# Kernel tuning notes

Measured on AMD Instinct MI355X. Metric: run time of the kernel, lower is better.

Reference implementation:

```python
import jax, jax.numpy as jnp
import numpy as np
from jax import lax

B, L, T, H = 8192, 1024, 32, 32  # batch, input length, time steps, lstm hidden
EPS = 1e-5


def _conv1d(x, w, stride, pad):
    # x: [N, C, L], w: [O, I, K]
    return lax.conv_general_dilated(x, w, (stride,), [(pad, pad)],
                                    dimension_numbers=('NCH', 'OIH', 'NCH'))


def _bn(x, g, be, m, v):
    # eval-mode batchnorm over channel dim of [N, C, L]
    inv = g / jnp.sqrt(v + EPS)
    return x * inv[None, :, None] + (be - m * inv)[None, :, None]


def setup_inputs() -> dict:
    key = jax.random.key(0)
    ks = jax.random.split(key, 32)
    r = lambda i, shape, s=0.1: jax.random.normal(ks[i], shape, jnp.float32) * s
    u = lambda i, shape: jax.random.uniform(ks[i], shape, jnp.float32, 0.5, 1.5)
    return {
        'x': jax.random.normal(ks[0], (B, L, 1), jnp.float32),
        'w1': r(1, (8, 1, 7)), 'b1': r(2, (8,)), 'g1': u(3, (8,)), 'be1': r(4, (8,)),
        'm1': r(5, (8,)), 'v1': u(6, (8,)),
        'w2': r(7, (16, 8, 5)), 'b2': r(8, (16,)), 'g2': u(9, (16,)), 'be2': r(10, (16,)),
        'm2': r(11, (16,)), 'v2': u(12, (16,)),
        'w3': r(13, (32, 16, 3)), 'b3': r(14, (32,)), 'g3': u(15, (32,)), 'be3': r(16, (32,)),
        'm3': r(17, (32,)), 'v3': u(18, (32,)),
        'w_ih': r(19, (4 * H, 32)), 'w_hh': r(20, (4 * H, H)),
        'b_ih': r(21, (4 * H,)), 'b_hh': r(22, (4 * H,)),
        'fc1w': r(23, (64, 64)), 'fc1b': r(24, (64,)),
        'fc2w': r(25, (32, 64)), 'fc2b': r(26, (32,)),
        'fc3w': r(27, (4, 32)), 'fc3b': r(28, (4,)),
    }


def _forward(x, w1, b1, g1, be1, m1, v1, w2, b2, g2, be2, m2, v2,
             w3, b3, g3, be3, m3, v3, w_ih, w_hh, b_ih, b_hh,
             fc1w, fc1b, fc2w, fc2b, fc3w, fc3b):
    bsz = x.shape[0]
    h = x.transpose(0, 2, 1)                      # [B, 1, 1024]
    h = jax.nn.relu(_bn(_conv1d(h, w1, 4, 3) + b1[None, :, None], g1, be1, m1, v1))
    h = jax.nn.relu(_bn(_conv1d(h, w2, 4, 2) + b2[None, :, None], g2, be2, m2, v2))
    h = jax.nn.relu(_bn(_conv1d(h, w3, 2, 1) + b3[None, :, None], g3, be3, m3, v3))
    # h: [B, 32, 32]
    spatial = h.mean(axis=2)                      # [B, 32]
    snn_in = h.transpose(0, 2, 1).reshape(bsz, T, -1)  # [B, 32, 32]

    # LIF neuron: sequential decay/threshold/reset scan over time
    def lif_step(mem, xt):
        mem = 0.9 * mem + xt
        spike = (mem > 0.5).astype(xt.dtype)
        mem = mem * (1.0 - spike)
        return mem, spike

    _, spikes = lax.scan(lif_step, jnp.zeros((bsz, snn_in.shape[2]), snn_in.dtype),
                         snn_in.transpose(1, 0, 2))  # spikes: [T, B, F]

    # single-layer LSTM, keep only last hidden state
    def lstm_step(carry, xt):
        hh, cc = carry
        gates = xt @ w_ih.T + b_ih + hh @ w_hh.T + b_hh
        i, f, g, o = jnp.split(gates, 4, axis=1)
        cc = jax.nn.sigmoid(f) * cc + jax.nn.sigmoid(i) * jnp.tanh(g)
        hh = jax.nn.sigmoid(o) * jnp.tanh(cc)
        return (hh, cc), None

    init = (jnp.zeros((bsz, H), x.dtype), jnp.zeros((bsz, H), x.dtype))
    (h_last, _), _ = lax.scan(lstm_step, init, spikes)

    combined = jnp.concatenate([h_last, spatial], axis=1)  # [B, 64]
    z = jax.nn.relu(combined @ fc1w.T + fc1b)
    z = jax.nn.relu(z @ fc2w.T + fc2b)
    out = z @ fc3w.T + fc3b                                # [B, 4]
    return out, spatial, h_last


def reference(x, w1, b1, g1, be1, m1, v1, w2, b2, g2, be2, m2, v2,
              w3, b3, g3, be3, m3, v3, w_ih, w_hh, b_ih, b_hh,
              fc1w, fc1b, fc2w, fc2b, fc3w, fc3b):
    return _forward(x, w1, b1, g1, be1, m1, v1, w2, b2, g2, be2, m2, v2,
                    w3, b3, g3, be3, m3, v3, w_ih, w_hh, b_ih, b_hh,
                    fc1w, fc1b, fc2w, fc2b, fc3w, fc3b)
```

## Files before the change

kernel.cpp:

```cpp
#include <hip/hip_runtime.h>

#define NB 8192
#define EPS_BN 1e-5f

#define PADX(i) ((i) + ((((i) >> 5)) << 2))

using bf16x8 = __attribute__((ext_vector_type(8))) __bf16;
using bf16x4 = __attribute__((ext_vector_type(4))) __bf16;
using f32x4  = __attribute__((ext_vector_type(4))) float;
using f32x2  = __attribute__((ext_vector_type(2))) float;
using u32x4  = __attribute__((ext_vector_type(4))) unsigned int;

#define WSF_OFF 262144
#define PK_WIH  2560
#define PK_WHH  4608
#define PK_FC1  6656
#define PK_FC2  8704
#define PK_FC3  9728
#define PK_BFR  9984
#define PK_B1   10112
#define PK_B2   10176
#define PK_B3   10208
#define PK_SPB  12288

__device__ inline unsigned pack_bf16(float a, float b) {
    union { __bf16 h; unsigned short u; } ca, cb;
    ca.h = (__bf16)a; cb.h = (__bf16)b;
    return (unsigned)ca.u | ((unsigned)cb.u << 16);
}

__global__ __launch_bounds__(256) void fold_kernel(
    const float* __restrict__ w1, const float* __restrict__ b1,
    const float* __restrict__ g1, const float* __restrict__ be1,
    const float* __restrict__ m1, const float* __restrict__ v1,
    const float* __restrict__ w2, const float* __restrict__ b2,
    const float* __restrict__ g2, const float* __restrict__ be2,
    const float* __restrict__ m2, const float* __restrict__ v2,
    const float* __restrict__ w3, const float* __restrict__ b3,
    const float* __restrict__ g3, const float* __restrict__ be3,
    const float* __restrict__ m3, const float* __restrict__ v3,
    const float* __restrict__ w_ih, const float* __restrict__ w_hh,
    const float* __restrict__ b_ih, const float* __restrict__ b_hh,
    const float* __restrict__ fc1w, const float* __restrict__ fc1b,
    const float* __restrict__ fc2w, const float* __restrict__ fc2b,
    const float* __restrict__ fc3w, const float* __restrict__ fc3b,
    float* __restrict__ wsf)
{
    int j = blockIdx.x * 256 + threadIdx.x;
    if (j < 64) {
        int k = j >> 3, c = j & 7;
        wsf[j] = (k < 7) ? w1[c * 7 + k] * (g1[c] * rsqrtf(v1[c] + EPS_BN)) : 0.f;
    } else if (j < 72) {
        int c = j - 64;
        float inv = g1[c] * rsqrtf(v1[c] + EPS_BN);
        wsf[j] = (b1[c] - m1[c]) * inv + be1[c];
    } else if (j >= 80 && j < 720) {
        int i = j - 80, c = i & 15, t = i >> 4, ci = t / 5, k = t - 5 * ci;
        wsf[j] = w2[(c * 8 + ci) * 5 + k] * (g2[c] * rsqrtf(v2[c] + EPS_BN));
    } else if (j >= 720 && j < 736) {
        int c = j - 720;
        float inv = g2[c] * rsqrtf(v2[c] + EPS_BN);
        wsf[j] = (b2[c] - m2[c]) * inv + be2[c];
    } else if (j >= 736 && j < 2272) {
        int i = j - 736, c = i & 31, t = i >> 5, ci = t / 3, k = t - 3 * ci;
        wsf[j] = w3[(c * 16 + ci) * 3 + k] * (g3[c] * rsqrtf(v3[c] + EPS_BN));
    } else if (j >= 2272 && j < 2304) {
        int c = j - 2272;
        float inv = g3[c] * rsqrtf(v3[c] + EPS_BN);
        wsf[j] = (b3[c] - m3[c]) * inv + be3[c];
    } else if (j >= 2560 && j < 3072) {
        int idx = j - 2560, T = idx >> 6, j6 = idx & 63, row = j6 & 15, q = j6 >> 4;
        const float* src = w_ih + (size_t)(16 * T + row) * 32 + 8 * q;
        unsigned* dst = (unsigned*)(wsf + PK_WIH) + (size_t)idx * 4;
        #pragma unroll
        for (int i = 0; i < 4; i++) dst[i] = pack_bf16(src[2 * i], src[2 * i + 1]);
    } else if (j >= 3072 && j < 3584) {
        int idx = j - 3072, T = idx >> 6, j6 = idx & 63, row = j6 & 15, q = j6 >> 4;
        const float* src = w_hh + (size_t)(16 * T + row) * 32 + 8 * q;
        unsigned* dst = (unsigned*)(wsf + PK_WHH) + (size_t)idx * 4;
        #pragma unroll
        for (int i = 0; i < 4; i++) dst[i] = pack_bf16(src[2 * i], src[2 * i + 1]);
    } else if (j >= 3584 && j < 4096) {
        int idx = j - 3584, f = idx >> 6, j6 = idx & 63, row = j6 & 15, q = j6 >> 4;
        int T = f >> 1, s = f & 1;
        const float* src = fc1w + (size_t)(16 * T + row) * 64 + 32 * s + 8 * q;
        unsigned* dst = (unsigned*)(wsf + PK_FC1) + (size_t)idx * 4;
        #pragma unroll
        for (int i = 0; i < 4; i++) dst[i] = pack_bf16(src[2 * i], src[2 * i + 1]);
    } else if (j >= 4096 && j < 4352) {
        int idx = j - 4096, f = idx >> 6, j6 = idx & 63, row = j6 & 15, q = j6 >> 4;
        int T = f >> 1, s = f & 1;
        const float* src = fc2w + (size_t)(16 * T + row) * 64 + 32 * s + 8 * q;
        unsigned* dst = (unsigned*)(wsf + PK_FC2) + (size_t)idx * 4;
        #pragma unroll
        for (int i = 0; i < 4; i++) dst[i] = pack_bf16(src[2 * i], src[2 * i + 1]);
    } else if (j >= 4352 && j < 4416) {
        int j6 = j - 4352, row = j6 & 15, q = j6 >> 4;
        const float* src = fc3w + (size_t)(row & 3) * 32 + 8 * q;
        unsigned* dst = (unsigned*)(wsf + PK_FC3) + (size_t)j6 * 4;
        #pragma unroll
        for (int i = 0; i < 4; i++) dst[i] = pack_bf16(src[2 * i], src[2 * i + 1]);
    } else if (j >= 4416 && j < 4448) {
        int idx = j - 4416, T = idx >> 2, q = idx & 3;
        #pragma unroll
        for (int i = 0; i < 4; i++)
            wsf[PK_BFR + idx * 4 + i] = b_ih[16 * T + 4 * q + i] + b_hh[16 * T + 4 * q + i];
    } else if (j >= 4448 && j < 4464) {
        int idx = j - 4448, T = idx >> 2, q = idx & 3;
        #pragma unroll
        for (int i = 0; i < 4; i++) wsf[PK_B1 + idx * 4 + i] = fc1b[16 * T + 4 * q + i];
    } else if (j >= 4464 && j < 4472) {
        int idx = j - 4464, T = idx >> 2, q = idx & 3;
        #pragma unroll
        for (int i = 0; i < 4; i++) wsf[PK_B2 + idx * 4 + i] = fc2b[16 * T + 4 * q + i];
    } else if (j == 4472) {
        #pragma unroll
        for (int i = 0; i < 4; i++) wsf[PK_B3 + i] = fc3b[i];
    }
}

__device__ inline f32x2 pkfma(f32x2 a, f32x2 b, f32x2 c) {
    return __builtin_elementwise_fma(a, b, c);
}

__device__ inline void conv1_pos(float* __restrict__ c1t,
                                 const float* __restrict__ xb,
                                 const float* __restrict__ wsf,
                                 int p, int idx)
{
    float4 gb = *reinterpret_cast<const float4*>(xb + 4 * p);
    float4 ga = make_float4(0.f, 0.f, 0.f, 0.f);
    if (p > 0) ga = *reinterpret_cast<const float4*>(xb + 4 * p - 4);
    float win[7] = {ga.y, ga.z, ga.w, gb.x, gb.y, gb.z, gb.w};
    #pragma unroll
    for (int cp = 0; cp < 4; cp++) {
        f32x2 acc = *reinterpret_cast<const f32x2*>(wsf + 64 + 2 * cp);
        #pragma unroll
        for (int k = 0; k < 7; k++) {
            f32x2 wv = *reinterpret_cast<const f32x2*>(wsf + k * 8 + 2 * cp);
            f32x2 sv = {win[k], win[k]};
            acc = pkfma(wv, sv, acc);
        }
        c1t[(2 * cp + 0) * 148 + PADX(idx)] = fmaxf(acc[0], 0.f);
        c1t[(2 * cp + 1) * 148 + PADX(idx)] = fmaxf(acc[1], 0.f);
    }
}

__global__ __launch_bounds__(256) void conv_lif_kernel(
    const float* __restrict__ x,
    float* __restrict__ wsf,
    float* __restrict__ spatial_out,
    unsigned int* __restrict__ spk)
{
    __shared__ alignas(16) float smem[4812];
    float* const c1b = smem;
    float* const c3b = smem;
    float* const c2b = smem + 2376;

    const int b0  = blockIdx.x * 2;
    const int tid = threadIdx.x;
    const float* xg0 = x + (size_t)b0 * 1024;
    const float* xg1 = x + (size_t)(b0 + 1) * 1024;

    #pragma unroll
    for (int h = 0; h < 2; h++) {
        {
            const int be = tid >> 7;
            const int lp = tid & 127;
            const float* xb = be ? xg1 : xg0;
            float* c1t = c1b + be * 1188;
            const int p = 126 * h + lp;
            conv1_pos(c1t, xb, wsf, p, p + 2 - 128 * h);
            if (h == 1 && lp == 0)
                conv1_pos(c1t, xb, wsf, 254, 128);
            if (h == 0 && lp < 2) {
                #pragma unroll
                for (int ch = 0; ch < 8; ch++) c1t[ch * 148 + lp] = 0.f;
            }
        }
        __syncthreads();

        {
            const int Pl = tid & 31;
            const int be = (tid >> 5) & 1;
            const int cq = __builtin_amdgcn_readfirstlane(tid >> 6) << 2;
            const int P  = 32 * h + Pl;
            const float* wB2 = wsf + 80;
            const float* bB2 = wsf + 720;
            f32x2 a01 = *reinterpret_cast<const f32x2*>(bB2 + cq);
            f32x2 a23 = *reinterpret_cast<const f32x2*>(bB2 + cq + 2);
            const float* c1t = c1b + be * 1188;
            float* c2t = c2b + be * 1220;
            if (h == 0 && Pl == 0) {
                #pragma unroll
                for (int j = 0; j < 4; j++) c2t[(cq + j) * 76] = 0.f;
            }
            #pragma unroll
            for (int ci = 0; ci < 8; ci++) {
                const float* row = c1t + ci * 148;
                float4 va = *reinterpret_cast<const float4*>(&row[PADX(4 * Pl)]);
                float  v4 = row[PADX(4 * Pl + 4)];
                float win[5] = {va.x, va.y, va.z, va.w, v4};
                #pragma unroll
                for (int k = 0; k < 5; k++) {
                    const float* wp = wB2 + (ci * 5 + k) * 16 + cq;
                    f32x2 sv = {win[k], win[k]};
                    a01 = pkfma(*reinterpret_cast<const f32x2*>(wp),     sv, a01);
                    a23 = pkfma(*reinterpret_cast<const f32x2*>(wp + 2), sv, a23);
                }
            }
            c2t[(cq + 0) * 76 + PADX(1 + P)] = fmaxf(a01[0], 0.f);
            c2t[(cq + 1) * 76 + PADX(1 + P)] = fmaxf(a01[1], 0.f);
            c2t[(cq + 2) * 76 + PADX(1 + P)] = fmaxf(a23[0], 0.f);
            c2t[(cq + 3) * 76 + PADX(1 + P)] = fmaxf(a23[1], 0.f);
        }
        __syncthreads();
    }

    {
        const int pl  = tid & 63;
        const int be  = pl >> 5;
        const int pos = pl & 31;
        const int cb  = __builtin_amdgcn_readfirstlane(tid >> 6) << 3;
        const float* wC3 = wsf + 736;
        const float* bC3 = wsf + 2272;
        f32x2 a01 = *reinterpret_cast<const f32x2*>(bC3 + cb);
        f32x2 a23 = *reinterpret_cast<const f32x2*>(bC3 + cb + 2);
        f32x2 a45 = *reinterpret_cast<const f32x2*>(bC3 + cb + 4);
        f32x2 a67 = *reinterpret_cast<const f32x2*>(bC3 + cb + 6);
        const float* c2t = c2b + be * 1220;
        #pragma unroll
        for (int ci = 0; ci < 16; ci++) {
            const float* row = c2t + ci * 76;
            float2 vab = *reinterpret_cast<const float2*>(&row[PADX(2 * pos)]);
            float  vc  = row[PADX(2 * pos + 2)];
            float win[3] = {vab.x, vab.y, vc};
            #pragma unroll
            for (int k = 0; k < 3; k++) {
                const float* wp = wC3 + (ci * 3 + k) * 32 + cb;
                f32x2 sv = {win[k], win[k]};
                a01 = pkfma(*reinterpret_cast<const f32x2*>(wp),     sv, a01);
                a23 = pkfma(*reinterpret_cast<const f32x2*>(wp + 2), sv, a23);
                a45 = pkfma(*reinterpret_cast<const f32x2*>(wp + 4), sv, a45);
                a67 = pkfma(*reinterpret_cast<const f32x2*>(wp + 6), sv, a67);
            }
        }
        float* c3t = c3b + be * 1060;
        c3t[(cb + 0) * 33 + pos] = fmaxf(a01[0], 0.f);
        c3t[(cb + 1) * 33 + pos] = fmaxf(a01[1], 0.f);
        c3t[(cb + 2) * 33 + pos] = fmaxf(a23[0], 0.f);
        c3t[(cb + 3) * 33 + pos] = fmaxf(a23[1], 0.f);
        c3t[(cb + 4) * 33 + pos] = fmaxf(a45[0], 0.f);
        c3t[(cb + 5) * 33 + pos] = fmaxf(a45[1], 0.f);
        c3t[(cb + 6) * 33 + pos] = fmaxf(a67[0], 0.f);
        c3t[(cb + 7) * 33 + pos] = fmaxf(a67[1], 0.f);
    }
    __syncthreads();

    if (tid < 64) {
        const int be = tid >> 5, ch = tid & 31;
        const float* c3t = c3b + be * 1060;
        float s = 0.f;
        #pragma unroll
        for (int t = 0; t < 32; t++) s += c3t[ch * 33 + t];
        float sv = s * 0.03125f;
        spatial_out[(size_t)(b0 + be) * 32 + ch] = sv;
        union { __bf16 h; unsigned short u; } cv;
        cv.h = (__bf16)sv;
        ((unsigned short*)(wsf + PK_SPB))[(size_t)(b0 + be) * 32 + ch] = cv.u;

        float mem = 0.f;
        #pragma unroll
        for (int t = 0; t < 32; t++) {
            mem = __fadd_rn(__fmul_rn(0.9f, mem), c3t[ch * 33 + t]);
            bool spike = mem > 0.5f;
            mem = spike ? 0.f : mem;
            unsigned long long msk = __ballot(spike);
            if (tid == 0) {
                spk[(size_t)b0 * 32 + t]      = (unsigned int)(msk & 0xffffffffull);
                spk[(size_t)b0 * 32 + 32 + t] = (unsigned int)(msk >> 32);
            }
        }
    }
}

__device__ inline float sigm(float x) {
    return __builtin_amdgcn_rcpf(1.f + __expf(-x));
}
__device__ inline float tanh_(float x) {
    return fmaf(2.f, __builtin_amdgcn_rcpf(1.f + __expf(-2.f * x)), -1.f);
}

__global__ __launch_bounds__(64, 2) void lstm_fc_mfma_kernel(
    const unsigned int* __restrict__ spk,
    const float* __restrict__ wsf,
    float* __restrict__ out0,
    float* __restrict__ hlast_out)
{
    const int l    = threadIdx.x;
    const int row  = l & 15;
    const int q    = l >> 4;
    const int base = blockIdx.x * 16;

    __shared__ unsigned int mlds[512];
    __shared__ __bf16 hlds[640];
    __shared__ __bf16 zlds[1152];

    for (int i = l; i < 512; i += 64) {
        int j = i >> 5, t = i & 31;
        mlds[t * 16 + j] = spk[(size_t)(base + j) * 32 + t];
    }
    for (int i = l; i < 640; i += 64) hlds[i] = (__bf16)0.f;

    union bc { u32x4 u; bf16x8 v; };
    const u32x4* wihp = (const u32x4*)(wsf + PK_WIH);
    const u32x4* whhp = (const u32x4*)(wsf + PK_WHH);

    bf16x8 wih[8], whh[8];
    f32x4  bfr[8];
    #pragma unroll
    for (int T = 0; T < 8; T++) {
        bc a; a.u = wihp[T * 64 + l]; wih[T] = a.v;
        bc b; b.u = whhp[T * 64 + l]; whh[T] = b.v;
        bfr[T] = *reinterpret_cast<const f32x4*>(wsf + PK_BFR + (T * 4 + q) * 4);
    }

    float cst[8], hq[8];
    #pragma unroll
    for (int i = 0; i < 8; i++) { cst[i] = 0.f; hq[i] = 0.f; }

    #pragma unroll 1
    for (int t = 0; t < 32; t++) {
        unsigned int m  = mlds[t * 16 + row];
        unsigned int by = (m >> (q * 8)) & 0xFFu;
        union { bf16x8 v; unsigned int u[4]; } a1;
        a1.u[0] = ((by & 1u)        * 0x3F80u) | (((by >> 1) & 1u) * 0x3F800000u);
        a1.u[1] = (((by >> 2) & 1u) * 0x3F80u) | (((by >> 3) & 1u) * 0x3F800000u);
        a1.u[2] = (((by >> 4) & 1u) * 0x3F80u) | (((by >> 5) & 1u) * 0x3F800000u);
        a1.u[3] = (((by >> 6) & 1u) * 0x3F80u) | (((by >> 7) & 1u) * 0x3F800000u);
        bf16x8 a2 = *reinterpret_cast<bf16x8*>(&hlds[row * 40 + q * 8]);

        f32x4 acc[8];
        #pragma unroll
        for (int T = 0; T < 8; T++) {
            acc[T] = __builtin_amdgcn_mfma_f32_16x16x32_bf16(wih[T], a1.v, bfr[T], 0, 0, 0);
            acc[T] = __builtin_amdgcn_mfma_f32_16x16x32_bf16(whh[T], a2,   acc[T], 0, 0, 0);
        }

        #pragma unroll
        for (int j = 0; j < 4; j++) {
            float iv = sigm(acc[0][j]);
            float fv = sigm(acc[2][j]);
            float gv = tanh_(acc[4][j]);
            float ov = sigm(acc[6][j]);
            cst[j] = fmaf(fv, cst[j], iv * gv);
            hq[j]  = ov * tanh_(cst[j]);
            float iv2 = sigm(acc[1][j]);
            float fv2 = sigm(acc[3][j]);
            float gv2 = tanh_(acc[5][j]);
            float ov2 = sigm(acc[7][j]);
            cst[4 + j] = fmaf(fv2, cst[4 + j], iv2 * gv2);
            hq[4 + j]  = ov2 * tanh_(cst[4 + j]);
        }

        bf16x4 hv0, hv1;
        #pragma unroll
        for (int j = 0; j < 4; j++) { hv0[j] = (__bf16)hq[j]; hv1[j] = (__bf16)hq[4 + j]; }
        *reinterpret_cast<bf16x4*>(&hlds[row * 40 + 4 * q])      = hv0;
        *reinterpret_cast<bf16x4*>(&hlds[row * 40 + 16 + 4 * q]) = hv1;
    }

    {
        f32x4 lo, hi;
        #pragma unroll
        for (int j = 0; j < 4; j++) { lo[j] = hq[j]; hi[j] = hq[4 + j]; }
        *reinterpret_cast<f32x4*>(hlast_out + (size_t)(base + row) * 32 + 4 * q)      = lo;
        *reinterpret_cast<f32x4*>(hlast_out + (size_t)(base + row) * 32 + 16 + 4 * q) = hi;
    }

    bf16x8 hf = *reinterpret_cast<bf16x8*>(&hlds[row * 40 + q * 8]);
    bf16x8 spf;
    {
        bc s_;
        s_.u = *reinterpret_cast<const u32x4*>(
            (const unsigned short*)(wsf + PK_SPB) + (size_t)(base + row) * 32 + 8 * q);
        spf = s_.v;
    }

    const u32x4* fc1p = (const u32x4*)(wsf + PK_FC1);
    #pragma unroll
    for (int T = 0; T < 4; T++) {
        bc x0_, x1_;
        x0_.u = fc1p[(T * 2 + 0) * 64 + l];
        x1_.u = fc1p[(T * 2 + 1) * 64 + l];
        f32x4 c = *reinterpret_cast<const f32x4*>(wsf + PK_B1 + (T * 4 + q) * 4);
        f32x4 a = __builtin_amdgcn_mfma_f32_16x16x32_bf16(x0_.v, hf,  c, 0, 0, 0);
        a       = __builtin_amdgcn_mfma_f32_16x16x32_bf16(x1_.v, spf, a, 0, 0, 0);
        bf16x4 zv;
        #pragma unroll
        for (int i = 0; i < 4; i++) zv[i] = (__bf16)fmaxf(a[i], 0.f);
        *reinterpret_cast<bf16x4*>(&zlds[row * 72 + 16 * T + 4 * q]) = zv;
    }
    bf16x8 z1f0 = *reinterpret_cast<bf16x8*>(&zlds[row * 72 + 8 * q]);
    bf16x8 z1f1 = *reinterpret_cast<bf16x8*>(&zlds[row * 72 + 32 + 8 * q]);

    const u32x4* fc2p = (const u32x4*)(wsf + PK_FC2);
    #pragma unroll
    for (int T = 0; T < 2; T++) {
        bc x0_, x1_;
        x0_.u = fc2p[(T * 2 + 0) * 64 + l];
        x1_.u = fc2p[(T * 2 + 1) * 64 + l];
        f32x4 c = *reinterpret_cast<const f32x4*>(wsf + PK_B2 + (T * 4 + q) * 4);
        f32x4 a = __builtin_amdgcn_mfma_f32_16x16x32_bf16(x0_.v, z1f0, c, 0, 0, 0);
        a       = __builtin_amdgcn_mfma_f32_16x16x32_bf16(x1_.v, z1f1, a, 0, 0, 0);
        bf16x4 zv;
        #pragma unroll
        for (int i = 0; i < 4; i++) zv[i] = (__bf16)fmaxf(a[i], 0.f);
        *reinterpret_cast<bf16x4*>(&hlds[row * 40 + 16 * T + 4 * q]) = zv;
    }
    bf16x8 z2f = *reinterpret_cast<bf16x8*>(&hlds[row * 40 + 8 * q]);

    {
        bc x3_;
        x3_.u = ((const u32x4*)(wsf + PK_FC3))[l];
        f32x4 c = *reinterpret_cast<const f32x4*>(wsf + PK_B3);
        f32x4 o = __builtin_amdgcn_mfma_f32_16x16x32_bf16(x3_.v, z2f, c, 0, 0, 0);
        if (l < 16)
            *reinterpret_cast<f32x4*>(out0 + (size_t)(base + row) * 4) = o;
    }
}

extern "C" void kernel_launch(void* const* d_in, const int* in_sizes, int n_in,
                              void* d_out, int out_size, void* d_ws, size_t ws_size,
                              hipStream_t stream) {
    const float* x    = (const float*)d_in[0];
    const float* w1   = (const float*)d_in[1];
    const float* b1   = (const float*)d_in[2];
    const float* g1   = (const float*)d_in[3];
    const float* be1  = (const float*)d_in[4];
    const float* m1   = (const float*)d_in[5];
    const float* v1   = (const float*)d_in[6];
    const float* w2   = (const float*)d_in[7];
    const float* b2   = (const float*)d_in[8];
    const float* g2   = (const float*)d_in[9];
    const float* be2  = (const float*)d_in[10];
    const float* m2   = (const float*)d_in[11];
    const float* v2   = (const float*)d_in[12];
    const float* w3   = (const float*)d_in[13];
    const float* b3   = (const float*)d_in[14];
    const float* g3   = (const float*)d_in[15];
    const float* be3  = (const float*)d_in[16];
    const float* m3   = (const float*)d_in[17];
    const float* v3   = (const float*)d_in[18];
    const float* w_ih = (const float*)d_in[19];
    const float* w_hh = (const float*)d_in[20];
    const float* b_ih = (const float*)d_in[21];
    const float* b_hh = (const float*)d_in[22];
    const float* fc1w = (const float*)d_in[23];
    const float* fc1b = (const float*)d_in[24];
    const float* fc2w = (const float*)d_in[25];
    const float* fc2b = (const float*)d_in[26];
    const float* fc3w = (const float*)d_in[27];
    const float* fc3b = (const float*)d_in[28];

    float* out0    = (float*)d_out;
    float* spatial = out0 + (size_t)NB * 4;
    float* hlast   = spatial + (size_t)NB * 32;
    unsigned int* spk = (unsigned int*)d_ws;
    float* wsf = (float*)d_ws + WSF_OFF;

    hipLaunchKernelGGL(fold_kernel, dim3(18), dim3(256), 0, stream,
                       w1, b1, g1, be1, m1, v1,
                       w2, b2, g2, be2, m2, v2,
                       w3, b3, g3, be3, m3, v3,
                       w_ih, w_hh, b_ih, b_hh,
                       fc1w, fc1b, fc2w, fc2b, fc3w, fc3b, wsf);

    hipLaunchKernelGGL(conv_lif_kernel, dim3(NB / 2), dim3(256), 0, stream,
                       x, wsf, spatial, spk);

    hipLaunchKernelGGL(lstm_fc_mfma_kernel, dim3(NB / 16), dim3(64), 0, stream,
                       spk, wsf, out0, hlast);
}
```

Baseline: 68.07 us.

## Process two independent 16-row LSTM tiles per wavefront to hide MFMA latency

Each LSTM wavefront now handles 32 batch rows as two independent 16-row tiles, interleaving their MFMA chains and gate math inside the sequential time loop. The aim is instruction-level parallelism: the serial dependency through h and c per step is latency-bound, and a second independent chain can fill MFMA and transcendental pipeline bubbles while weight registers are reused. In exchange the grid is halved to 256 single-wave blocks, which lowers the number of waves per CU on a large GPU. Register pressure also roughly doubles, and launch bounds are relaxed to allow it.

New measurement: 90.30 us. 32.7% more time.

```diff
diff --git a/kernel.cpp b/kernel.cpp
--- a/kernel.cpp
+++ b/kernel.cpp
@@ -291,7 +291,15 @@
     return fmaf(2.f, __builtin_amdgcn_rcpf(1.f + __expf(-2.f * x)), -1.f);
 }
 
-__global__ __launch_bounds__(64, 2) void lstm_fc_mfma_kernel(
+#define BUILD_A1(a1, m, q) do {                                              \
+    unsigned by_ = ((m) >> ((q) * 8)) & 0xFFu;                               \
+    (a1).u[0] = ((by_ & 1u)        * 0x3F80u) | (((by_ >> 1) & 1u) * 0x3F800000u); \
+    (a1).u[1] = (((by_ >> 2) & 1u) * 0x3F80u) | (((by_ >> 3) & 1u) * 0x3F800000u); \
+    (a1).u[2] = (((by_ >> 4) & 1u) * 0x3F80u) | (((by_ >> 5) & 1u) * 0x3F800000u); \
+    (a1).u[3] = (((by_ >> 6) & 1u) * 0x3F80u) | (((by_ >> 7) & 1u) * 0x3F800000u); \
+} while (0)
+
+__global__ __launch_bounds__(64, 1) void lstm_fc_mfma_kernel(
     const unsigned int* __restrict__ spk,
     const float* __restrict__ wsf,
     float* __restrict__ out0,
@@ -300,17 +308,17 @@
     const int l    = threadIdx.x;
     const int row  = l & 15;
     const int q    = l >> 4;
-    const int base = blockIdx.x * 16;
-
-    __shared__ unsigned int mlds[512];
-    __shared__ __bf16 hlds[640];
-    __shared__ __bf16 zlds[1152];
-
-    for (int i = l; i < 512; i += 64) {
-        int j = i >> 5, t = i & 31;
-        mlds[t * 16 + j] = spk[(size_t)(base + j) * 32 + t];
-    }
-    for (int i = l; i < 640; i += 64) hlds[i] = (__bf16)0.f;
+    const int base = blockIdx.x * 32;
+
+    __shared__ unsigned int mlds[1024];
+    __shared__ __bf16 hlds[1280];
+    __shared__ __bf16 zlds[2304];
+
+    for (int i = l; i < 1024; i += 64) {
+        int u = i >> 9, r = i & 511, j = r >> 5, t = r & 31;
+        mlds[u * 512 + t * 16 + j] = spk[(size_t)(base + u * 16 + j) * 32 + t];
+    }
+    for (int i = l; i < 1280; i += 64) hlds[i] = (__bf16)0.f;
 
     union bc { u32x4 u; bf16x8 v; };
     const u32x4* wihp = (const u32x4*)(wsf + PK_WIH);
@@ -325,108 +333,144 @@
         bfr[T] = *reinterpret_cast<const f32x4*>(wsf + PK_BFR + (T * 4 + q) * 4);
     }
 
-    float cst[8], hq[8];
+    float cstA[8], hqA[8], cstB[8], hqB[8];
     #pragma unroll
-    for (int i = 0; i < 8; i++) { cst[i] = 0.f; hq[i] = 0.f; }
+    for (int i = 0; i < 8; i++) { cstA[i] = 0.f; hqA[i] = 0.f; cstB[i] = 0.f; hqB[i] = 0.f; }
 
     #pragma unroll 1
     for (int t = 0; t < 32; t++) {
-        unsigned int m  = mlds[t * 16 + row];
-        unsigned int by = (m >> (q * 8)) & 0xFFu;
-        union { bf16x8 v; unsigned int u[4]; } a1;
-        a1.u[0] = ((by & 1u)        * 0x3F80u) | (((by >> 1) & 1u) * 0x3F800000u);
-        a1.u[1] = (((by >> 2) & 1u) * 0x3F80u) | (((by >> 3) & 1u) * 0x3F800000u);
-        a1.u[2] = (((by >> 4) & 1u) * 0x3F80u) | (((by >> 5) & 1u) * 0x3F800000u);
-        a1.u[3] = (((by >> 6) & 1u) * 0x3F80u) | (((by >> 7) & 1u) * 0x3F800000u);
-        bf16x8 a2 = *reinterpret_cast<bf16x8*>(&hlds[row * 40 + q * 8]);
-
-        f32x4 acc[8];
+        unsigned mA = mlds[t * 16 + row];
+        unsigned mB = mlds[512 + t * 16 + row];
+        union { bf16x8 v; unsigned u[4]; } a1A, a1B;
+        BUILD_A1(a1A, mA, q);
+        BUILD_A1(a1B, mB, q);
+        bf16x8 a2A = *reinterpret_cast<bf16x8*>(&hlds[row * 40 + q * 8]);
+        bf16x8 a2B = *reinterpret_cast<bf16x8*>(&hlds[640 + row * 40 + q * 8]);
+
+        f32x4 accA[8], accB[8];
         #pragma unroll
         for (int T = 0; T < 8; T++) {
-            acc[T] = __builtin_amdgcn_mfma_f32_16x16x32_bf16(wih[T], a1.v, bfr[T], 0, 0, 0);
-            acc[T] = __builtin_amdgcn_mfma_f32_16x16x32_bf16(whh[T], a2,   acc[T], 0, 0, 0);
+            accA[T] = __builtin_amdgcn_mfma_f32_16x16x32_bf16(wih[T], a1A.v, bfr[T], 0, 0, 0);
+            accB[T] = __builtin_amdgcn_mfma_f32_16x16x32_bf16(wih[T], a1B.v, bfr[T], 0, 0, 0);
+        }
+        #pragma unroll
+        for (int T = 0; T < 8; T++) {
+            accA[T] = __builtin_amdgcn_mfma_f32_16x16x32_bf16(whh[T], a2A, accA[T], 0, 0, 0);
+            accB[T] = __builtin_amdgcn_mfma_f32_16x16x32_bf16(whh[T], a2B, accB[T], 0, 0, 0);
         }
 
         #pragma unroll
         for (int j = 0; j < 4; j++) {
-            float iv = sigm(acc[0][j]);
-            float fv = sigm(acc[2][j]);
-            float gv = tanh_(acc[4][j]);
-            float ov = sigm(acc[6][j]);
-            cst[j] = fmaf(fv, cst[j], iv * gv);
-            hq[j]  = ov * tanh_(cst[j]);
-            float iv2 = sigm(acc[1][j]);
-            float fv2 = sigm(acc[3][j]);
-            float gv2 = tanh_(acc[5][j]);
-            float ov2 = sigm(acc[7][j]);
-            cst[4 + j] = fmaf(fv2, cst[4 + j], iv2 * gv2);
-            hq[4 + j]  = ov2 * tanh_(cst[4 + j]);
-        }
-
-        bf16x4 hv0, hv1;
-        #pragma unroll
-        for (int j = 0; j < 4; j++) { hv0[j] = (__bf16)hq[j]; hv1[j] = (__bf16)hq[4 + j]; }
-        *reinterpret_cast<bf16x4*>(&hlds[row * 40 + 4 * q])      = hv0;
-        *reinterpret_cast<bf16x4*>(&hlds[row * 40 + 16 + 4 * q]) = hv1;
+            {
+                float iv = sigm(accA[0][j]);
+                float fv = sigm(accA[2][j]);
+                float gv = tanh_(accA[4][j]);
+                float ov = sigm(accA[6][j]);
+                cstA[j] = fmaf(fv, cstA[j], iv * gv);
+                hqA[j]  = ov * tanh_(cstA[j]);
+                float iv2 = sigm(accA[1][j]);
+                float fv2 = sigm(accA[3][j]);
+                float gv2 = tanh_(accA[5][j]);
+                float ov2 = sigm(accA[7][j]);
+                cstA[4 + j] = fmaf(fv2, cstA[4 + j], iv2 * gv2);
+                hqA[4 + j]  = ov2 * tanh_(cstA[4 + j]);
+            }
+            {
+                float iv = sigm(accB[0][j]);
+                float fv = sigm(accB[2][j]);
+                float gv = tanh_(accB[4][j]);
+                float ov = sigm(accB[6][j]);
+                cstB[j] = fmaf(fv, cstB[j], iv * gv);
+                hqB[j]  = ov * tanh_(cstB[j]);
+                float iv2 = sigm(accB[1][j]);
+                float fv2 = sigm(accB[3][j]);
+                float gv2 = tanh_(accB[5][j]);
+                float ov2 = sigm(accB[7][j]);
+                cstB[4 + j] = fmaf(fv2, cstB[4 + j], iv2 * gv2);
+                hqB[4 + j]  = ov2 * tanh_(cstB[4 + j]);
+            }
+        }
+
+        bf16x4 hv0A, hv1A, hv0B, hv1B;
+        #pragma unroll
+        for (int j = 0; j < 4; j++) {
+            hv0A[j] = (__bf16)hqA[j]; hv1A[j] = (__bf16)hqA[4 + j];
+            hv0B[j] = (__bf16)hqB[j]; hv1B[j] = (__bf16)hqB[4 + j];
+        }
+        *reinterpret_cast<bf16x4*>(&hlds[row * 40 + 4 * q])            = hv0A;
+        *reinterpret_cast<bf16x4*>(&hlds[row * 40 + 16 + 4 * q])       = hv1A;
+        *reinterpret_cast<bf16x4*>(&hlds[640 + row * 40 + 4 * q])      = hv0B;
+        *reinterpret_cast<bf16x4*>(&hlds[640 + row * 40 + 16 + 4 * q]) = hv1B;
     }
 
     {
         f32x4 lo, hi;
         #pragma unroll
-        for (int j = 0; j < 4; j++) { lo[j] = hq[j]; hi[j] = hq[4 + j]; }
+        for (int j = 0; j < 4; j++) { lo[j] = hqA[j]; hi[j] = hqA[4 + j]; }
         *reinterpret_cast<f32x4*>(hlast_out + (size_t)(base + row) * 32 + 4 * q)      = lo;
         *reinterpret_cast<f32x4*>(hlast_out + (size_t)(base + row) * 32 + 16 + 4 * q) = hi;
-    }
-
-    bf16x8 hf = *reinterpret_cast<bf16x8*>(&hlds[row * 40 + q * 8]);
-    bf16x8 spf;
-    {
-        bc s_;
-        s_.u = *reinterpret_cast<const u32x4*>(
-            (const unsigned short*)(wsf + PK_SPB) + (size_t)(base + row) * 32 + 8 * q);
-        spf = s_.v;
+        #pragma unroll
+        for (int j = 0; j < 4; j++) { lo[j] = hqB[j]; hi[j] = hqB[4 + j]; }
+        *reinterpret_cast<f32x4*>(hlast_out + (size_t)(base + 16 + row) * 32 + 4 * q)      = lo;
+        *reinterpret_cast<f32x4*>(hlast_out + (size_t)(base + 16 + row) * 32 + 16 + 4 * q) = hi;
     }
 
     const u32x4* fc1p = (const u32x4*)(wsf + PK_FC1);
-    #pragma unroll
-    for (int T = 0; T < 4; T++) {
-        bc x0_, x1_;
-        x0_.u = fc1p[(T * 2 + 0) * 64 + l];
-        x1_.u = fc1p[(T * 2 + 1) * 64 + l];
-        f32x4 c = *reinterpret_cast<const f32x4*>(wsf + PK_B1 + (T * 4 + q) * 4);
-        f32x4 a = __builtin_amdgcn_mfma_f32_16x16x32_bf16(x0_.v, hf,  c, 0, 0, 0);
-        a       = __builtin_amdgcn_mfma_f32_16x16x32_bf16(x1_.v, spf, a, 0, 0, 0);
-        bf16x4 zv;
-        #pragma unroll
-        for (int i = 0; i < 4; i++) zv[i] = (__bf16)fmaxf(a[i], 0.f);
-        *reinterpret_cast<bf16x4*>(&zlds[row * 72 + 16 * T + 4 * q]) = zv;
-    }
-    bf16x8 z1f0 = *reinterpret_cast<bf16x8*>(&zlds[row * 72 + 8 * q]);
-    bf16x8 z1f1 = *reinterpret_cast<bf16x8*>(&zlds[row * 72 + 32 + 8 * q]);
-
     const u32x4* fc2p = (const u32x4*)(wsf + PK_FC2);
     #pragma unroll
-    for (int T = 0; T < 2; T++) {
-        bc x0_, x1_;
-        x0_.u = fc2p[(T * 2 + 0) * 64 + l];
-        x1_.u = fc2p[(T * 2 + 1) * 64 + l];
-        f32x4 c = *reinterpret_cast<const f32x4*>(wsf + PK_B2 + (T * 4 + q) * 4);
-        f32x4 a = __builtin_amdgcn_mfma_f32_16x16x32_bf16(x0_.v, z1f0, c, 0, 0, 0);
-        a       = __builtin_amdgcn_mfma_f32_16x16x32_bf16(x1_.v, z1f1, a, 0, 0, 0);
-        bf16x4 zv;
-        #pragma unroll
-        for (int i = 0; i < 4; i++) zv[i] = (__bf16)fmaxf(a[i], 0.f);
-        *reinterpret_cast<bf16x4*>(&hlds[row * 40 + 16 * T + 4 * q]) = zv;
-    }
-    bf16x8 z2f = *reinterpret_cast<bf16x8*>(&hlds[row * 40 + 8 * q]);
-
-    {
-        bc x3_;
-        x3_.u = ((const u32x4*)(wsf + PK_FC3))[l];
-        f32x4 c = *reinterpret_cast<const f32x4*>(wsf + PK_B3);
-        f32x4 o = __builtin_amdgcn_mfma_f32_16x16x32_bf16(x3_.v, z2f, c, 0, 0, 0);
-        if (l < 16)
-            *reinterpret_cast<f32x4*>(out0 + (size_t)(base + row) * 4) = o;
+    for (int u = 0; u < 2; u++) {
+        __bf16* hl = hlds + u * 640;
+        __bf16* zl = zlds + u * 1152;
+        const int tb = base + u * 16;
+
+        bf16x8 hf = *reinterpret_cast<bf16x8*>(&hl[row * 40 + 8 * q]);
+        bf16x8 spf;
+        {
+            bc s_;
+            s_.u = *reinterpret_cast<const u32x4*>(
+                (const unsigned short*)(wsf + PK_SPB) + (size_t)(tb + row) * 32 + 8 * q);
+            spf = s_.v;
+        }
+
+        #pragma unroll
+        for (int T = 0; T < 4; T++) {
+            bc x0_, x1_;
+            x0_.u = fc1p[(T * 2 + 0) * 64 + l];
+            x1_.u = fc1p[(T * 2 + 1) * 64 + l];
+            f32x4 c = *reinterpret_cast<const f32x4*>(wsf + PK_B1 + (T * 4 + q) * 4);
+            f32x4 a = __builtin_amdgcn_mfma_f32_16x16x32_bf16(x0_.v, hf,  c, 0, 0, 0);
+            a       = __builtin_amdgcn_mfma_f32_16x16x32_bf16(x1_.v, spf, a, 0, 0, 0);
+            bf16x4 zv;
+            #pragma unroll
+            for (int i = 0; i < 4; i++) zv[i] = (__bf16)fmaxf(a[i], 0.f);
+            *reinterpret_cast<bf16x4*>(&zl[row * 72 + 16 * T + 4 * q]) = zv;
+        }
+        bf16x8 z1f0 = *reinterpret_cast<bf16x8*>(&zl[row * 72 + 8 * q]);
+        bf16x8 z1f1 = *reinterpret_cast<bf16x8*>(&zl[row * 72 + 32 + 8 * q]);
+
+        #pragma unroll
+        for (int T = 0; T < 2; T++) {
+            bc x0_, x1_;
+            x0_.u = fc2p[(T * 2 + 0) * 64 + l];
+            x1_.u = fc2p[(T * 2 + 1) * 64 + l];
+            f32x4 c = *reinterpret_cast<const f32x4*>(wsf + PK_B2 + (T * 4 + q) * 4);
+            f32x4 a = __builtin_amdgcn_mfma_f32_16x16x32_bf16(x0_.v, z1f0, c, 0, 0, 0);
+            a       = __builtin_amdgcn_mfma_f32_16x16x32_bf16(x1_.v, z1f1, a, 0, 0, 0);
+            bf16x4 zv;
+            #pragma unroll
+            for (int i = 0; i < 4; i++) zv[i] = (__bf16)fmaxf(a[i], 0.f);
+            *reinterpret_cast<bf16x4*>(&hl[row * 40 + 16 * T + 4 * q]) = zv;
+        }
+        bf16x8 z2f = *reinterpret_cast<bf16x8*>(&hl[row * 40 + 8 * q]);
+
+        {
+            bc x3_;
+            x3_.u = ((const u32x4*)(wsf + PK_FC3))[l];
+            f32x4 c = *reinterpret_cast<const f32x4*>(wsf + PK_B3);
+            f32x4 o = __builtin_amdgcn_mfma_f32_16x16x32_bf16(x3_.v, z2f, c, 0, 0, 0);
+            if (l < 16)
+                *reinterpret_cast<f32x4*>(out0 + (size_t)(tb + row) * 4) = o;
+        }
     }
 }
 
@@ -479,6 +523,6 @@
     hipLaunchKernelGGL(conv_lif_kernel, dim3(NB / 2), dim3(256), 0, stream,
                        x, wsf, spatial, spk);
 
-    hipLaunchKernelGGL(lstm_fc_mfma_kernel, dim3(NB / 16), dim3(64), 0, stream,
+    hipLaunchKernelGGL(lstm_fc_mfma_kernel, dim3(NB / 32), dim3(64), 0, stream,
                        spk, wsf, out0, hlast);
 }
```

## Split LSTM gate tiles across two wavefronts with double-buffered hidden state

Applied to the files above, without the earlier changes.

The LSTM+FC kernel now runs two wavefronts per 16-row block, each computing half of the gate tiles (one 16-column half of the hidden state), so each wave does half the MFMAs and activations per step. The hidden state is double-buffered in LDS with a block barrier per time step so both halves exchange h. The FC layers are likewise split between the waves. This shortens the serial per-step latency chain, at the cost of 32 extra barriers per block and more threads per block.

New measurement: 67.74 us. About the same (-0.5%).

```diff
diff --git a/kernel.cpp b/kernel.cpp
--- a/kernel.cpp
+++ b/kernel.cpp
@@ -291,44 +291,49 @@
     return fmaf(2.f, __builtin_amdgcn_rcpf(1.f + __expf(-2.f * x)), -1.f);
 }
 
-__global__ __launch_bounds__(64, 2) void lstm_fc_mfma_kernel(
+__global__ __launch_bounds__(128, 2) void lstm_fc_mfma_kernel(
     const unsigned int* __restrict__ spk,
     const float* __restrict__ wsf,
     float* __restrict__ out0,
     float* __restrict__ hlast_out)
 {
-    const int l    = threadIdx.x;
+    const int ltid = threadIdx.x;
+    const int l    = ltid & 63;
+    const int w    = ltid >> 6;
     const int row  = l & 15;
     const int q    = l >> 4;
     const int base = blockIdx.x * 16;
 
     __shared__ unsigned int mlds[512];
-    __shared__ __bf16 hlds[640];
-    __shared__ __bf16 zlds[1152];
-
-    for (int i = l; i < 512; i += 64) {
+    __shared__ alignas(16) __bf16 hdb[2][640];
+    __shared__ alignas(16) __bf16 zlds[1152];
+
+    for (int i = ltid; i < 512; i += 128) {
         int j = i >> 5, t = i & 31;
         mlds[t * 16 + j] = spk[(size_t)(base + j) * 32 + t];
     }
-    for (int i = l; i < 640; i += 64) hlds[i] = (__bf16)0.f;
+    for (int i = ltid; i < 640; i += 128) hdb[0][i] = (__bf16)0.f;
 
     union bc { u32x4 u; bf16x8 v; };
     const u32x4* wihp = (const u32x4*)(wsf + PK_WIH);
     const u32x4* whhp = (const u32x4*)(wsf + PK_WHH);
 
-    bf16x8 wih[8], whh[8];
-    f32x4  bfr[8];
+    bf16x8 wih[4], whh[4];
+    f32x4  bfr[4];
     #pragma unroll
-    for (int T = 0; T < 8; T++) {
-        bc a; a.u = wihp[T * 64 + l]; wih[T] = a.v;
-        bc b; b.u = whhp[T * 64 + l]; whh[T] = b.v;
-        bfr[T] = *reinterpret_cast<const f32x4*>(wsf + PK_BFR + (T * 4 + q) * 4);
-    }
-
-    float cst[8], hq[8];
+    for (int g = 0; g < 4; g++) {
+        const int T = 2 * g + w;
+        bc a; a.u = wihp[T * 64 + l]; wih[g] = a.v;
+        bc b; b.u = whhp[T * 64 + l]; whh[g] = b.v;
+        bfr[g] = *reinterpret_cast<const f32x4*>(wsf + PK_BFR + (T * 4 + q) * 4);
+    }
+
+    float cst[4], hq[4];
     #pragma unroll
-    for (int i = 0; i < 8; i++) { cst[i] = 0.f; hq[i] = 0.f; }
-
+    for (int i = 0; i < 4; i++) { cst[i] = 0.f; hq[i] = 0.f; }
+    __syncthreads();
+
+    int cur = 0;
     #pragma unroll 1
     for (int t = 0; t < 32; t++) {
         unsigned int m  = mlds[t * 16 + row];
@@ -338,47 +343,41 @@
         a1.u[1] = (((by >> 2) & 1u) * 0x3F80u) | (((by >> 3) & 1u) * 0x3F800000u);
         a1.u[2] = (((by >> 4) & 1u) * 0x3F80u) | (((by >> 5) & 1u) * 0x3F800000u);
         a1.u[3] = (((by >> 6) & 1u) * 0x3F80u) | (((by >> 7) & 1u) * 0x3F800000u);
-        bf16x8 a2 = *reinterpret_cast<bf16x8*>(&hlds[row * 40 + q * 8]);
-
-        f32x4 acc[8];
-        #pragma unroll
-        for (int T = 0; T < 8; T++) {
-            acc[T] = __builtin_amdgcn_mfma_f32_16x16x32_bf16(wih[T], a1.v, bfr[T], 0, 0, 0);
-            acc[T] = __builtin_amdgcn_mfma_f32_16x16x32_bf16(whh[T], a2,   acc[T], 0, 0, 0);
+        bf16x8 a2 = *reinterpret_cast<bf16x8*>(&hdb[cur][row * 40 + q * 8]);
+
+        f32x4 acc[4];
+        #pragma unroll
+        for (int g = 0; g < 4; g++) {
+            acc[g] = __builtin_amdgcn_mfma_f32_16x16x32_bf16(wih[g], a1.v, bfr[g], 0, 0, 0);
+            acc[g] = __builtin_amdgcn_mfma_f32_16x16x32_bf16(whh[g], a2,   acc[g], 0, 0, 0);
         }
 
         #pragma unroll
         for (int j = 0; j < 4; j++) {
             float iv = sigm(acc[0][j]);
-            float fv = sigm(acc[2][j]);
-            float gv = tanh_(acc[4][j]);
-            float ov = sigm(acc[6][j]);
+            float fv = sigm(acc[1][j]);
+            float gv = tanh_(acc[2][j]);
+            float ov = sigm(acc[3][j]);
             cst[j] = fmaf(fv, cst[j], iv * gv);
             hq[j]  = ov * tanh_(cst[j]);
-            float iv2 = sigm(acc[1][j]);
-            float fv2 = sigm(acc[3][j]);
-            float gv2 = tanh_(acc[5][j]);
-            float ov2 = sigm(acc[7][j]);
-            cst[4 + j] = fmaf(fv2, cst[4 + j], iv2 * gv2);
-            hq[4 + j]  = ov2 * tanh_(cst[4 + j]);
-        }
-
-        bf16x4 hv0, hv1;
-        #pragma unroll
-        for (int j = 0; j < 4; j++) { hv0[j] = (__bf16)hq[j]; hv1[j] = (__bf16)hq[4 + j]; }
-        *reinterpret_cast<bf16x4*>(&hlds[row * 40 + 4 * q])      = hv0;
-        *reinterpret_cast<bf16x4*>(&hlds[row * 40 + 16 + 4 * q]) = hv1;
+        }
+
+        bf16x4 hv;
+        #pragma unroll
+        for (int j = 0; j < 4; j++) hv[j] = (__bf16)hq[j];
+        *reinterpret_cast<bf16x4*>(&hdb[cur ^ 1][row * 40 + 16 * w + 4 * q]) = hv;
+        __syncthreads();
+        cur ^= 1;
     }
 
     {
-        f32x4 lo, hi;
-        #pragma unroll
-        for (int j = 0; j < 4; j++) { lo[j] = hq[j]; hi[j] = hq[4 + j]; }
-        *reinterpret_cast<f32x4*>(hlast_out + (size_t)(base + row) * 32 + 4 * q)      = lo;
-        *reinterpret_cast<f32x4*>(hlast_out + (size_t)(base + row) * 32 + 16 + 4 * q) = hi;
-    }
-
-    bf16x8 hf = *reinterpret_cast<bf16x8*>(&hlds[row * 40 + q * 8]);
+        f32x4 lo;
+        #pragma unroll
+        for (int j = 0; j < 4; j++) lo[j] = hq[j];
+        *reinterpret_cast<f32x4*>(hlast_out + (size_t)(base + row) * 32 + 16 * w + 4 * q) = lo;
+    }
+
+    bf16x8 hf = *reinterpret_cast<bf16x8*>(&hdb[cur][row * 40 + 8 * q]);
     bf16x8 spf;
     {
         bc s_;
@@ -389,7 +388,8 @@
 
     const u32x4* fc1p = (const u32x4*)(wsf + PK_FC1);
     #pragma unroll
-    for (int T = 0; T < 4; T++) {
+    for (int g = 0; g < 2; g++) {
+        const int T = 2 * g + w;
         bc x0_, x1_;
         x0_.u = fc1p[(T * 2 + 0) * 64 + l];
         x1_.u = fc1p[(T * 2 + 1) * 64 + l];
@@ -401,12 +401,13 @@
         for (int i = 0; i < 4; i++) zv[i] = (__bf16)fmaxf(a[i], 0.f);
         *reinterpret_cast<bf16x4*>(&zlds[row * 72 + 16 * T + 4 * q]) = zv;
     }
+    __syncthreads();
     bf16x8 z1f0 = *reinterpret_cast<bf16x8*>(&zlds[row * 72 + 8 * q]);
     bf16x8 z1f1 = *reinterpret_cast<bf16x8*>(&zlds[row * 72 + 32 + 8 * q]);
 
     const u32x4* fc2p = (const u32x4*)(wsf + PK_FC2);
-    #pragma unroll
-    for (int T = 0; T < 2; T++) {
+    {
+        const int T = w;
         bc x0_, x1_;
         x0_.u = fc2p[(T * 2 + 0) * 64 + l];
         x1_.u = fc2p[(T * 2 + 1) * 64 + l];
@@ -416,11 +417,12 @@
         bf16x4 zv;
         #pragma unroll
         for (int i = 0; i < 4; i++) zv[i] = (__bf16)fmaxf(a[i], 0.f);
-        *reinterpret_cast<bf16x4*>(&hlds[row * 40 + 16 * T + 4 * q]) = zv;
-    }
-    bf16x8 z2f = *reinterpret_cast<bf16x8*>(&hlds[row * 40 + 8 * q]);
-
-    {
+        *reinterpret_cast<bf16x4*>(&hdb[cur ^ 1][row * 40 + 16 * T + 4 * q]) = zv;
+    }
+    __syncthreads();
+
+    if (w == 0) {
+        bf16x8 z2f = *reinterpret_cast<bf16x8*>(&hdb[cur ^ 1][row * 40 + 8 * q]);
         bc x3_;
         x3_.u = ((const u32x4*)(wsf + PK_FC3))[l];
         f32x4 c = *reinterpret_cast<const f32x4*>(wsf + PK_B3);
@@ -479,6 +481,6 @@
     hipLaunchKernelGGL(conv_lif_kernel, dim3(NB / 2), dim3(256), 0, stream,
                        x, wsf, spatial, spk);
 
-    hipLaunchKernelGGL(lstm_fc_mfma_kernel, dim3(NB / 16), dim3(64), 0, stream,
+    hipLaunchKernelGGL(lstm_fc_mfma_kernel, dim3(NB / 16), dim3(128), 0, stream,
                        spk, wsf, out0, hlast);
 }
```
